# Optimization experiments

Hardware: AMD Instinct MI355X
Metric: run time of the kernel (lower is better)

Reference implementation:

```python
import jax, jax.numpy as jnp
import numpy as np

F_DIM = 128
H_DIM = 64
N_NODES = 100000
N_EDGES = 1000000
BN_EPS = 1e-5

def setup_inputs() -> dict:
    key = jax.random.key(0)
    ks = jax.random.split(key, 10)
    x = jax.random.normal(ks[0], (N_NODES, F_DIM), dtype=jnp.float32)
    edges = jax.random.randint(ks[1], (2, N_EDGES), 0, N_NODES, dtype=jnp.int64)
    s_in = 1.0 / np.sqrt(2 * F_DIM)
    s_h = 1.0 / np.sqrt(H_DIM)
    W_in = jax.random.uniform(ks[2], (H_DIM, 2 * F_DIM), jnp.float32, -s_in, s_in)
    b_in = jax.random.uniform(ks[3], (H_DIM,), jnp.float32, -s_in, s_in)
    W_h = jax.random.uniform(ks[4], (H_DIM, H_DIM), jnp.float32, -s_h, s_h)
    b_h = jax.random.uniform(ks[5], (H_DIM,), jnp.float32, -s_h, s_h)
    gamma = jnp.ones((H_DIM,), jnp.float32)
    beta = jnp.zeros((H_DIM,), jnp.float32)
    W_out = jax.random.uniform(ks[6], (1, H_DIM), jnp.float32, -s_h, s_h)
    b_out = jax.random.uniform(ks[7], (1,), jnp.float32, -s_h, s_h)
    return {"x": x, "edges": edges, "W_in": W_in, "b_in": b_in,
            "W_h": W_h, "b_h": b_h, "gamma": gamma, "beta": beta,
            "W_out": W_out, "b_out": b_out}

def reference(x, edges, W_in, b_in, W_h, b_h, gamma, beta, W_out, b_out):
    # gather node pair features and concat -> [E, 2F]
    ef = jnp.concatenate((x[edges[0]], x[edges[1]]), axis=1)
    h = jax.nn.relu(ef @ W_in.T + b_in)          # [E, H]
    h = h @ W_h.T + b_h                           # hidden linear
    # BatchNorm1d in training mode: batch stats over edge dim (biased var)
    mean = jnp.mean(h, axis=0)
    var = jnp.mean((h - mean) ** 2, axis=0)
    h = (h - mean) * jax.lax.rsqrt(var + BN_EPS) * gamma + beta
    h = jax.nn.relu(h)
    edge_scores = (h @ W_out.T + b_out).squeeze(-1)  # [E]
    return edge_scores
```

## Files before the change

### kernel.cpp

```cpp
#include <hip/hip_runtime.h>
#include <hip/hip_bf16.h>

#define N_NODES 100000
#define N_EDGES 1000000
#define BN_EPS 1e-5f
#define N_CHUNKS (N_EDGES / 64)

typedef __attribute__((ext_vector_type(8))) short bf16x8;
typedef __attribute__((ext_vector_type(4))) float f32x4;


__device__ __forceinline__ unsigned pk2(float a, float b) {
  unsigned ua = __builtin_bit_cast(unsigned, a);
  unsigned ub = __builtin_bit_cast(unsigned, b);
  ua += 0x7fffu + ((ua >> 16) & 1u);
  ub += 0x7fffu + ((ub >> 16) & 1u);
  return (ua >> 16) | (ub & 0xffff0000u);
}

__device__ __forceinline__ bf16x8 pack8(float4 v0, float4 v1) {
  uint4 u = make_uint4(pk2(v0.x, v0.y), pk2(v0.z, v0.w), pk2(v1.x, v1.y), pk2(v1.z, v1.w));
  return __builtin_bit_cast(bf16x8, u);
}

__global__ __launch_bounds__(64) void k_probe(const unsigned* __restrict__ eu,
                                              int* __restrict__ flag) {
  if (threadIdx.x == 0) {
    unsigned acc = 0;
#pragma unroll
    for (int i = 1; i < 64; i += 2) acc |= eu[i];
    *flag = (acc == 0) ? 1 : 0;
  }
}

__global__ __launch_bounds__(256) void k1_mfma(
    const float* __restrict__ x, const float* __restrict__ W_in,
    const float* __restrict__ b_in, __hip_bfloat16* __restrict__ A,
    float* __restrict__ stats) {
  const int t = threadIdx.x;
  if (blockIdx.x == 0 && t < 128) stats[t] = 0.f;
  const int lane = t & 63;
  const int w = t >> 6;
  const int l15 = lane & 15, l4 = lane >> 4;
  const int nb = blockIdx.x * 128 + (w >> 1) * 64;
  const int cb = (w & 1) * 64;

  bf16x8 wfrag[4][4];
#pragma unroll
  for (int ct = 0; ct < 4; ++ct) {
#pragma unroll
    for (int kk = 0; kk < 4; ++kk) {
      const float* wp = W_in + (16 * ct + l15) * 256 + (cb ? 128 : 0) + 32 * kk + 8 * l4;
      wfrag[ct][kk] = pack8(*(const float4*)wp, *(const float4*)(wp + 4));
    }
  }
  f32x4 acc[4][4];
#pragma unroll
  for (int nt = 0; nt < 4; ++nt)
#pragma unroll
    for (int ct = 0; ct < 4; ++ct)
      acc[nt][ct] = (f32x4){0.f, 0.f, 0.f, 0.f};

#pragma unroll
  for (int nt = 0; nt < 4; ++nt) {
    int node = nb + 16 * nt + l15;
    node = node < N_NODES ? node : N_NODES - 1;
    const float* xr = x + (size_t)node * 128 + 8 * l4;
#pragma unroll
    for (int kk = 0; kk < 4; ++kk) {
      const bf16x8 xf = pack8(*(const float4*)(xr + 32 * kk), *(const float4*)(xr + 32 * kk + 4));
#pragma unroll
      for (int ct = 0; ct < 4; ++ct)
        acc[nt][ct] = __builtin_amdgcn_mfma_f32_16x16x32_bf16(wfrag[ct][kk], xf, acc[nt][ct], 0, 0, 0);
    }
  }

  float4 bv[4];
#pragma unroll
  for (int ct = 0; ct < 4; ++ct)
    bv[ct] = cb ? make_float4(0.f, 0.f, 0.f, 0.f) : *(const float4*)(b_in + 16 * ct + 4 * l4);
#pragma unroll
  for (int nt = 0; nt < 4; ++nt) {
    const int node = nb + 16 * nt + l15;
    if (node < N_NODES) {
      __hip_bfloat16* ap = A + (size_t)node * 128 + cb + 4 * l4;
#pragma unroll
      for (int ct = 0; ct < 4; ++ct) {
        uint2 u;
        u.x = pk2(acc[nt][ct][0] + bv[ct].x, acc[nt][ct][1] + bv[ct].y);
        u.y = pk2(acc[nt][ct][2] + bv[ct].z, acc[nt][ct][3] + bv[ct].w);
        *(uint2*)(ap + 16 * ct) = u;
      }
    }
  }
}


__device__ __forceinline__ void stage_wh(const float* __restrict__ W_h, uint4* btile) {
  const int t = threadIdx.x;
#pragma unroll
  for (int rep = 0; rep < 2; ++rep) {
    const int idx = t + rep * 256;
    const int row = idx >> 3, c = idx & 7;
    const float* wp = W_h + row * 64 + c * 8;
    const float4 w0 = *(const float4*)wp;
    const float4 w1 = *(const float4*)(wp + 4);
    btile[row * 8 + (c ^ (row & 7))] =
        make_uint4(pk2(w0.x, w0.y), pk2(w0.z, w0.w), pk2(w1.x, w1.y), pk2(w1.z, w1.w));
  }
}

__device__ __forceinline__ void stage_h1(const __hip_bfloat16* __restrict__ As,
                                         const __hip_bfloat16* __restrict__ Ad,
                                         uint4* mytile, int lane) {
  const uint4* pa = (const uint4*)As;
  const uint4* pd = (const uint4*)Ad;
#pragma unroll
  for (int c = 0; c < 8; ++c) {
    const uint4 a = pa[c], d = pd[c];
    uint4 r;
    const unsigned* aw = (const unsigned*)&a;
    const unsigned* dw = (const unsigned*)&d;
    unsigned* rw = (unsigned*)&r;
#pragma unroll
    for (int q = 0; q < 4; ++q) {
      const float alo = __builtin_bit_cast(float, aw[q] << 16);
      const float ahi = __builtin_bit_cast(float, aw[q] & 0xffff0000u);
      const float dlo = __builtin_bit_cast(float, dw[q] << 16);
      const float dhi = __builtin_bit_cast(float, dw[q] & 0xffff0000u);
      rw[q] = pk2(fmaxf(alo + dlo, 0.f), fmaxf(ahi + dhi, 0.f));
    }
    mytile[lane * 8 + (c ^ (lane & 7))] = r;
  }
}

__global__ __launch_bounds__(256) void k2_stats(
    const __hip_bfloat16* __restrict__ A, const void* __restrict__ edges,
    const int* __restrict__ flag, const float* __restrict__ W_h,
    float* __restrict__ stats) {
  __shared__ uint4 tiles[4][64 * 8];
  __shared__ uint4 btile[64 * 8];
  const int lane = threadIdx.x & 63;
  const int wid = threadIdx.x >> 6;
  const int l15 = lane & 15, l4 = lane >> 4, lsw = l15 & 7;
  uint4* mytile = tiles[wid];
  stage_wh(W_h, btile);
  __syncthreads();
  bf16x8 bfr[4][2];
#pragma unroll
  for (int nt = 0; nt < 4; ++nt)
#pragma unroll
    for (int kk = 0; kk < 2; ++kk)
      bfr[nt][kk] = __builtin_bit_cast(bf16x8,
          btile[(nt * 16 + l15) * 8 + ((kk * 4 + l4) ^ lsw)]);

  const int is64 = *flag;
  const long long* e64 = (const long long*)edges;
  const int* e32 = (const int*)edges;
  float vs[4] = {0.f, 0.f, 0.f, 0.f};
  float vq[4] = {0.f, 0.f, 0.f, 0.f};
  const int gwave = blockIdx.x * 4 + wid;
  const int nwaves = gridDim.x * 4;
  for (int chunk = gwave; chunk < N_CHUNKS; chunk += nwaves) {
    const int e = chunk * 64 + lane;
    int s, d;
    if (is64) { s = (int)e64[e]; d = (int)e64[N_EDGES + e]; }
    else      { s = e32[e];      d = e32[N_EDGES + e]; }
    stage_h1(A + (size_t)s * 128, A + (size_t)d * 128 + 64, mytile, lane);
    asm volatile("s_waitcnt lgkmcnt(0)" ::: "memory");
    __builtin_amdgcn_sched_barrier(0);
#pragma unroll
    for (int mt = 0; mt < 4; ++mt) {
      const int arow = (mt * 16 + l15) * 8;
      const bf16x8 a0 = __builtin_bit_cast(bf16x8, mytile[arow + ((l4) ^ lsw)]);
      const bf16x8 a1 = __builtin_bit_cast(bf16x8, mytile[arow + ((4 + l4) ^ lsw)]);
#pragma unroll
      for (int nt = 0; nt < 4; ++nt) {
        f32x4 cacc = {0.f, 0.f, 0.f, 0.f};
        cacc = __builtin_amdgcn_mfma_f32_16x16x32_bf16(a0, bfr[nt][0], cacc, 0, 0, 0);
        cacc = __builtin_amdgcn_mfma_f32_16x16x32_bf16(a1, bfr[nt][1], cacc, 0, 0, 0);
#pragma unroll
        for (int j = 0; j < 4; ++j) {
          vs[nt] += cacc[j];
          vq[nt] += cacc[j] * cacc[j];
        }
      }
    }
  }
#pragma unroll
  for (int nt = 0; nt < 4; ++nt) {
    float s1 = vs[nt], s2 = vq[nt];
    s1 += __shfl_xor(s1, 16, 64); s1 += __shfl_xor(s1, 32, 64);
    s2 += __shfl_xor(s2, 16, 64); s2 += __shfl_xor(s2, 32, 64);
    if (lane < 16) {
      atomicAdd(&stats[lane + 16 * nt], s1);
      atomicAdd(&stats[64 + lane + 16 * nt], s2);
    }
  }
}

__global__ __launch_bounds__(64) void k3_finalize(
    const float* __restrict__ stats, const float* __restrict__ gamma,
    const float* __restrict__ beta, float* __restrict__ ss) {
  const int c = threadIdx.x;
  if (c < 64) {
    const float inv_e = 1.f / (float)N_EDGES;
    const float mg = stats[c] * inv_e;
    const float var = stats[64 + c] * inv_e - mg * mg;
    const float scale = gamma[c] * rsqrtf(var + BN_EPS);
    ss[c] = scale;
    ss[64 + c] = beta[c] - scale * mg;
  }
}

__global__ __launch_bounds__(256) void k4_out(
    const __hip_bfloat16* __restrict__ A, const void* __restrict__ edges,
    const int* __restrict__ flag, const float* __restrict__ W_h,
    const float* __restrict__ ss, const float* __restrict__ W_out,
    const float* __restrict__ b_out, float* __restrict__ out) {
  __shared__ uint4 tiles[4][64 * 8];
  __shared__ uint4 btile[64 * 8];
  const int lane = threadIdx.x & 63;
  const int wid = threadIdx.x >> 6;
  const int l15 = lane & 15, l4 = lane >> 4, lsw = l15 & 7;
  uint4* mytile = tiles[wid];
  stage_wh(W_h, btile);
  __syncthreads();
  bf16x8 bfr[4][2];
#pragma unroll
  for (int nt = 0; nt < 4; ++nt)
#pragma unroll
    for (int kk = 0; kk < 2; ++kk)
      bfr[nt][kk] = __builtin_bit_cast(bf16x8,
          btile[(nt * 16 + l15) * 8 + ((kk * 4 + l4) ^ lsw)]);
  float scl[4], shf[4], wo[4];
#pragma unroll
  for (int nt = 0; nt < 4; ++nt) {
    scl[nt] = ss[l15 + 16 * nt];
    shf[nt] = ss[64 + l15 + 16 * nt];
    wo[nt] = W_out[l15 + 16 * nt];
  }
  const float bo = b_out[0];
  const int is64 = *flag;
  const long long* e64 = (const long long*)edges;
  const int* e32 = (const int*)edges;
  const int gwave = blockIdx.x * 4 + wid;
  const int nwaves = gridDim.x * 4;
  for (int chunk = gwave; chunk < N_CHUNKS; chunk += nwaves) {
    const int e = chunk * 64 + lane;
    int s, d;
    if (is64) { s = (int)e64[e]; d = (int)e64[N_EDGES + e]; }
    else      { s = e32[e];      d = e32[N_EDGES + e]; }
    stage_h1(A + (size_t)s * 128, A + (size_t)d * 128 + 64, mytile, lane);
    asm volatile("s_waitcnt lgkmcnt(0)" ::: "memory");
    __builtin_amdgcn_sched_barrier(0);
#pragma unroll
    for (int mt = 0; mt < 4; ++mt) {
      const int arow = (mt * 16 + l15) * 8;
      const bf16x8 a0 = __builtin_bit_cast(bf16x8, mytile[arow + ((l4) ^ lsw)]);
      const bf16x8 a1 = __builtin_bit_cast(bf16x8, mytile[arow + ((4 + l4) ^ lsw)]);
      float t0 = 0.f, t1 = 0.f, t2 = 0.f, t3 = 0.f;
#pragma unroll
      for (int nt = 0; nt < 4; ++nt) {
        f32x4 cacc = {0.f, 0.f, 0.f, 0.f};
        cacc = __builtin_amdgcn_mfma_f32_16x16x32_bf16(a0, bfr[nt][0], cacc, 0, 0, 0);
        cacc = __builtin_amdgcn_mfma_f32_16x16x32_bf16(a1, bfr[nt][1], cacc, 0, 0, 0);
        t0 += fmaxf(fmaf(cacc[0], scl[nt], shf[nt]), 0.f) * wo[nt];
        t1 += fmaxf(fmaf(cacc[1], scl[nt], shf[nt]), 0.f) * wo[nt];
        t2 += fmaxf(fmaf(cacc[2], scl[nt], shf[nt]), 0.f) * wo[nt];
        t3 += fmaxf(fmaf(cacc[3], scl[nt], shf[nt]), 0.f) * wo[nt];
      }
      const int ebase = chunk * 64 + mt * 16 + 4 * l4;
#pragma unroll
      for (int j = 0; j < 4; ++j) {
        float r = (j == 0) ? t0 : (j == 1) ? t1 : (j == 2) ? t2 : t3;
        r += __shfl_xor(r, 1, 64);
        r += __shfl_xor(r, 2, 64);
        r += __shfl_xor(r, 4, 64);
        r += __shfl_xor(r, 8, 64);
        if (l15 == 0) out[ebase + j] = r + bo;
      }
    }
  }
}

extern "C" void kernel_launch(void* const* d_in, const int* in_sizes, int n_in,
                              void* d_out, int out_size, void* d_ws, size_t ws_size,
                              hipStream_t stream) {
  const float* x     = (const float*)d_in[0];
  const void*  edges = d_in[1];
  const float* W_in  = (const float*)d_in[2];
  const float* b_in  = (const float*)d_in[3];
  const float* W_h   = (const float*)d_in[4];
  const float* gamma = (const float*)d_in[6];
  const float* beta  = (const float*)d_in[7];
  const float* W_out = (const float*)d_in[8];
  const float* b_out = (const float*)d_in[9];
  float* out = (float*)d_out;

  char* base = (char*)d_ws;
  __hip_bfloat16* A = (__hip_bfloat16*)base;
  float* stats = (float*)(base + (size_t)N_NODES * 128 * sizeof(__hip_bfloat16));
  float* ss    = stats + 128;
  int*   flag  = (int*)(ss + 128);

  k_probe<<<1, 64, 0, stream>>>((const unsigned*)edges, flag);
  k1_mfma<<<782, 256, 0, stream>>>(x, W_in, b_in, A, stats);
  k2_stats<<<1024, 256, 0, stream>>>(A, edges, flag, W_h, stats);
  k3_finalize<<<1, 64, 0, stream>>>(stats, gamma, beta, ss);
  k4_out<<<1024, 256, 0, stream>>>(A, edges, flag, W_h, ss, W_out, b_out, out);
}
```

Before: 243.4 us.

## Materialize hidden pre-BN activations in fp16 and stream them in output pass

The stats kernel now writes the hidden-layer MFMA outputs to workspace as fp16, so the output kernel can stream them instead of re-gathering node rows and redoing the matmul. Both gather kernels also drop the shared-memory staging of the A fragments and W_h, loading them straight from global memory into MFMA registers. This trades a second random gather plus matmul for a 128 MB write and a read of the intermediate. It adds fp16 rounding of the pre-BN values, and it falls back to the old path when the workspace is too small.

New measurement: 219.9 us. -9.6%, faster.

```diff
diff --git a/kernel.cpp b/kernel.cpp
--- a/kernel.cpp
+++ b/kernel.cpp
@@ -1,5 +1,6 @@
 #include <hip/hip_runtime.h>
 #include <hip/hip_bf16.h>
+#include <hip/hip_fp16.h>
 
 #define N_NODES 100000
 #define N_EDGES 1000000
@@ -21,6 +22,33 @@
 __device__ __forceinline__ bf16x8 pack8(float4 v0, float4 v1) {
   uint4 u = make_uint4(pk2(v0.x, v0.y), pk2(v0.z, v0.w), pk2(v1.x, v1.y), pk2(v1.z, v1.w));
   return __builtin_bit_cast(bf16x8, u);
+}
+
+__device__ __forceinline__ bf16x8 frag_relu_add(uint4 a, uint4 d) {
+  uint4 r;
+  const unsigned* aw = (const unsigned*)&a;
+  const unsigned* dw = (const unsigned*)&d;
+  unsigned* rw = (unsigned*)&r;
+#pragma unroll
+  for (int q = 0; q < 4; ++q) {
+    const float alo = __builtin_bit_cast(float, aw[q] << 16);
+    const float ahi = __builtin_bit_cast(float, aw[q] & 0xffff0000u);
+    const float dlo = __builtin_bit_cast(float, dw[q] << 16);
+    const float dhi = __builtin_bit_cast(float, dw[q] & 0xffff0000u);
+    rw[q] = pk2(fmaxf(alo + dlo, 0.f), fmaxf(ahi + dhi, 0.f));
+  }
+  return __builtin_bit_cast(bf16x8, r);
+}
+
+__device__ __forceinline__ void load_bfr(const float* __restrict__ W_h, int l15, int l4,
+                                         bf16x8 bfr[4][2]) {
+#pragma unroll
+  for (int nt = 0; nt < 4; ++nt)
+#pragma unroll
+    for (int kk = 0; kk < 2; ++kk) {
+      const float* wp = W_h + (16 * nt + l15) * 64 + (kk * 4 + l4) * 8;
+      bfr[nt][kk] = pack8(*(const float4*)wp, *(const float4*)(wp + 4));
+    }
 }
 
 __global__ __launch_bounds__(64) void k_probe(const unsigned* __restrict__ eu,
@@ -95,94 +123,54 @@
   }
 }
 
-
-__device__ __forceinline__ void stage_wh(const float* __restrict__ W_h, uint4* btile) {
-  const int t = threadIdx.x;
-#pragma unroll
-  for (int rep = 0; rep < 2; ++rep) {
-    const int idx = t + rep * 256;
-    const int row = idx >> 3, c = idx & 7;
-    const float* wp = W_h + row * 64 + c * 8;
-    const float4 w0 = *(const float4*)wp;
-    const float4 w1 = *(const float4*)(wp + 4);
-    btile[row * 8 + (c ^ (row & 7))] =
-        make_uint4(pk2(w0.x, w0.y), pk2(w0.z, w0.w), pk2(w1.x, w1.y), pk2(w1.z, w1.w));
-  }
-}
-
-__device__ __forceinline__ void stage_h1(const __hip_bfloat16* __restrict__ As,
-                                         const __hip_bfloat16* __restrict__ Ad,
-                                         uint4* mytile, int lane) {
-  const uint4* pa = (const uint4*)As;
-  const uint4* pd = (const uint4*)Ad;
-#pragma unroll
-  for (int c = 0; c < 8; ++c) {
-    const uint4 a = pa[c], d = pd[c];
-    uint4 r;
-    const unsigned* aw = (const unsigned*)&a;
-    const unsigned* dw = (const unsigned*)&d;
-    unsigned* rw = (unsigned*)&r;
-#pragma unroll
-    for (int q = 0; q < 4; ++q) {
-      const float alo = __builtin_bit_cast(float, aw[q] << 16);
-      const float ahi = __builtin_bit_cast(float, aw[q] & 0xffff0000u);
-      const float dlo = __builtin_bit_cast(float, dw[q] << 16);
-      const float dhi = __builtin_bit_cast(float, dw[q] & 0xffff0000u);
-      rw[q] = pk2(fmaxf(alo + dlo, 0.f), fmaxf(ahi + dhi, 0.f));
-    }
-    mytile[lane * 8 + (c ^ (lane & 7))] = r;
-  }
-}
-
+template<bool STORE_G>
 __global__ __launch_bounds__(256) void k2_stats(
     const __hip_bfloat16* __restrict__ A, const void* __restrict__ edges,
     const int* __restrict__ flag, const float* __restrict__ W_h,
-    float* __restrict__ stats) {
-  __shared__ uint4 tiles[4][64 * 8];
-  __shared__ uint4 btile[64 * 8];
+    float* __restrict__ stats, __half* __restrict__ g) {
   const int lane = threadIdx.x & 63;
-  const int wid = threadIdx.x >> 6;
-  const int l15 = lane & 15, l4 = lane >> 4, lsw = l15 & 7;
-  uint4* mytile = tiles[wid];
-  stage_wh(W_h, btile);
-  __syncthreads();
+  const int l15 = lane & 15, l4 = lane >> 4;
   bf16x8 bfr[4][2];
-#pragma unroll
-  for (int nt = 0; nt < 4; ++nt)
-#pragma unroll
-    for (int kk = 0; kk < 2; ++kk)
-      bfr[nt][kk] = __builtin_bit_cast(bf16x8,
-          btile[(nt * 16 + l15) * 8 + ((kk * 4 + l4) ^ lsw)]);
+  load_bfr(W_h, l15, l4, bfr);
 
   const int is64 = *flag;
   const long long* e64 = (const long long*)edges;
   const int* e32 = (const int*)edges;
   float vs[4] = {0.f, 0.f, 0.f, 0.f};
   float vq[4] = {0.f, 0.f, 0.f, 0.f};
-  const int gwave = blockIdx.x * 4 + wid;
+  const int gwave = blockIdx.x * 4 + (threadIdx.x >> 6);
   const int nwaves = gridDim.x * 4;
   for (int chunk = gwave; chunk < N_CHUNKS; chunk += nwaves) {
-    const int e = chunk * 64 + lane;
-    int s, d;
-    if (is64) { s = (int)e64[e]; d = (int)e64[N_EDGES + e]; }
-    else      { s = e32[e];      d = e32[N_EDGES + e]; }
-    stage_h1(A + (size_t)s * 128, A + (size_t)d * 128 + 64, mytile, lane);
-    asm volatile("s_waitcnt lgkmcnt(0)" ::: "memory");
-    __builtin_amdgcn_sched_barrier(0);
+    const int base = chunk * 64;
 #pragma unroll
     for (int mt = 0; mt < 4; ++mt) {
-      const int arow = (mt * 16 + l15) * 8;
-      const bf16x8 a0 = __builtin_bit_cast(bf16x8, mytile[arow + ((l4) ^ lsw)]);
-      const bf16x8 a1 = __builtin_bit_cast(bf16x8, mytile[arow + ((4 + l4) ^ lsw)]);
+      const int eidx = base + mt * 16 + l15;
+      int s, d;
+      if (is64) { s = (int)e64[eidx]; d = (int)e64[N_EDGES + eidx]; }
+      else      { s = e32[eidx];      d = e32[N_EDGES + eidx]; }
+      const uint4* As = (const uint4*)(A + (size_t)s * 128);
+      const uint4* Ad = (const uint4*)(A + (size_t)d * 128 + 64);
+      const uint4 as0 = As[l4], as1 = As[4 + l4];
+      const uint4 ad0 = Ad[l4], ad1 = Ad[4 + l4];
+      const bf16x8 a0 = frag_relu_add(as0, ad0);
+      const bf16x8 a1 = frag_relu_add(as1, ad1);
 #pragma unroll
       for (int nt = 0; nt < 4; ++nt) {
-        f32x4 cacc = {0.f, 0.f, 0.f, 0.f};
-        cacc = __builtin_amdgcn_mfma_f32_16x16x32_bf16(a0, bfr[nt][0], cacc, 0, 0, 0);
-        cacc = __builtin_amdgcn_mfma_f32_16x16x32_bf16(a1, bfr[nt][1], cacc, 0, 0, 0);
+        f32x4 c = {0.f, 0.f, 0.f, 0.f};
+        c = __builtin_amdgcn_mfma_f32_16x16x32_bf16(a0, bfr[nt][0], c, 0, 0, 0);
+        c = __builtin_amdgcn_mfma_f32_16x16x32_bf16(a1, bfr[nt][1], c, 0, 0, 0);
+        if (STORE_G) {
+          const __half2 h0 = __floats2half2_rn(c[0], c[1]);
+          const __half2 h1 = __floats2half2_rn(c[2], c[3]);
+          uint2 u;
+          u.x = __builtin_bit_cast(unsigned, h0);
+          u.y = __builtin_bit_cast(unsigned, h1);
+          *(uint2*)(g + ((((size_t)chunk * 4 + mt) * 4 + nt) * 64 + lane) * 4) = u;
+        }
 #pragma unroll
         for (int j = 0; j < 4; ++j) {
-          vs[nt] += cacc[j];
-          vq[nt] += cacc[j] * cacc[j];
+          vs[nt] += c[j];
+          vq[nt] += c[j] * c[j];
         }
       }
     }
@@ -213,26 +201,59 @@
   }
 }
 
-__global__ __launch_bounds__(256) void k4_out(
+__global__ __launch_bounds__(256) void k4_stream(
+    const __half* __restrict__ g, const float* __restrict__ ss,
+    const float* __restrict__ W_out, const float* __restrict__ b_out,
+    float* __restrict__ out) {
+  const int lane = threadIdx.x & 63;
+  const int l15 = lane & 15, l4 = lane >> 4;
+  float scl[4], shf[4], wo[4];
+#pragma unroll
+  for (int nt = 0; nt < 4; ++nt) {
+    scl[nt] = ss[l15 + 16 * nt];
+    shf[nt] = ss[64 + l15 + 16 * nt];
+    wo[nt] = W_out[l15 + 16 * nt];
+  }
+  const float bo = b_out[0];
+  const int gwave = blockIdx.x * 4 + (threadIdx.x >> 6);
+  const int nwaves = gridDim.x * 4;
+  for (int chunk = gwave; chunk < N_CHUNKS; chunk += nwaves) {
+#pragma unroll
+    for (int mt = 0; mt < 4; ++mt) {
+      float t0 = 0.f, t1 = 0.f, t2 = 0.f, t3 = 0.f;
+#pragma unroll
+      for (int nt = 0; nt < 4; ++nt) {
+        const uint2 u = *(const uint2*)(g + ((((size_t)chunk * 4 + mt) * 4 + nt) * 64 + lane) * 4);
+        const __half2 h0 = __builtin_bit_cast(__half2, u.x);
+        const __half2 h1 = __builtin_bit_cast(__half2, u.y);
+        t0 += fmaxf(fmaf(__low2float(h0),  scl[nt], shf[nt]), 0.f) * wo[nt];
+        t1 += fmaxf(fmaf(__high2float(h0), scl[nt], shf[nt]), 0.f) * wo[nt];
+        t2 += fmaxf(fmaf(__low2float(h1),  scl[nt], shf[nt]), 0.f) * wo[nt];
+        t3 += fmaxf(fmaf(__high2float(h1), scl[nt], shf[nt]), 0.f) * wo[nt];
+      }
+      const int ebase = chunk * 64 + mt * 16 + 4 * l4;
+#pragma unroll
+      for (int j = 0; j < 4; ++j) {
+        float r = (j == 0) ? t0 : (j == 1) ? t1 : (j == 2) ? t2 : t3;
+        r += __shfl_xor(r, 1, 64);
+        r += __shfl_xor(r, 2, 64);
+        r += __shfl_xor(r, 4, 64);
+        r += __shfl_xor(r, 8, 64);
+        if (l15 == 0) out[ebase + j] = r + bo;
+      }
+    }
+  }
+}
+
+__global__ __launch_bounds__(256) void k4_gather(
     const __hip_bfloat16* __restrict__ A, const void* __restrict__ edges,
     const int* __restrict__ flag, const float* __restrict__ W_h,
     const float* __restrict__ ss, const float* __restrict__ W_out,
     const float* __restrict__ b_out, float* __restrict__ out) {
-  __shared__ uint4 tiles[4][64 * 8];
-  __shared__ uint4 btile[64 * 8];
   const int lane = threadIdx.x & 63;
-  const int wid = threadIdx.x >> 6;
-  const int l15 = lane & 15, l4 = lane >> 4, lsw = l15 & 7;
-  uint4* mytile = tiles[wid];
-  stage_wh(W_h, btile);
-  __syncthreads();
+  const int l15 = lane & 15, l4 = lane >> 4;
   bf16x8 bfr[4][2];
-#pragma unroll
-  for (int nt = 0; nt < 4; ++nt)
-#pragma unroll
-    for (int kk = 0; kk < 2; ++kk)
-      bfr[nt][kk] = __builtin_bit_cast(bf16x8,
-          btile[(nt * 16 + l15) * 8 + ((kk * 4 + l4) ^ lsw)]);
+  load_bfr(W_h, l15, l4, bfr);
   float scl[4], shf[4], wo[4];
 #pragma unroll
   for (int nt = 0; nt < 4; ++nt) {
@@ -244,33 +265,32 @@
   const int is64 = *flag;
   const long long* e64 = (const long long*)edges;
   const int* e32 = (const int*)edges;
-  const int gwave = blockIdx.x * 4 + wid;
+  const int gwave = blockIdx.x * 4 + (threadIdx.x >> 6);
   const int nwaves = gridDim.x * 4;
   for (int chunk = gwave; chunk < N_CHUNKS; chunk += nwaves) {
-    const int e = chunk * 64 + lane;
-    int s, d;
-    if (is64) { s = (int)e64[e]; d = (int)e64[N_EDGES + e]; }
-    else      { s = e32[e];      d = e32[N_EDGES + e]; }
-    stage_h1(A + (size_t)s * 128, A + (size_t)d * 128 + 64, mytile, lane);
-    asm volatile("s_waitcnt lgkmcnt(0)" ::: "memory");
-    __builtin_amdgcn_sched_barrier(0);
+    const int base = chunk * 64;
 #pragma unroll
     for (int mt = 0; mt < 4; ++mt) {
-      const int arow = (mt * 16 + l15) * 8;
-      const bf16x8 a0 = __builtin_bit_cast(bf16x8, mytile[arow + ((l4) ^ lsw)]);
-      const bf16x8 a1 = __builtin_bit_cast(bf16x8, mytile[arow + ((4 + l4) ^ lsw)]);
+      const int eidx = base + mt * 16 + l15;
+      int s, d;
+      if (is64) { s = (int)e64[eidx]; d = (int)e64[N_EDGES + eidx]; }
+      else      { s = e32[eidx];      d = e32[N_EDGES + eidx]; }
+      const uint4* As = (const uint4*)(A + (size_t)s * 128);
+      const uint4* Ad = (const uint4*)(A + (size_t)d * 128 + 64);
+      const bf16x8 a0 = frag_relu_add(As[l4], Ad[l4]);
+      const bf16x8 a1 = frag_relu_add(As[4 + l4], Ad[4 + l4]);
       float t0 = 0.f, t1 = 0.f, t2 = 0.f, t3 = 0.f;
 #pragma unroll
       for (int nt = 0; nt < 4; ++nt) {
-        f32x4 cacc = {0.f, 0.f, 0.f, 0.f};
-        cacc = __builtin_amdgcn_mfma_f32_16x16x32_bf16(a0, bfr[nt][0], cacc, 0, 0, 0);
-        cacc = __builtin_amdgcn_mfma_f32_16x16x32_bf16(a1, bfr[nt][1], cacc, 0, 0, 0);
-        t0 += fmaxf(fmaf(cacc[0], scl[nt], shf[nt]), 0.f) * wo[nt];
-        t1 += fmaxf(fmaf(cacc[1], scl[nt], shf[nt]), 0.f) * wo[nt];
-        t2 += fmaxf(fmaf(cacc[2], scl[nt], shf[nt]), 0.f) * wo[nt];
-        t3 += fmaxf(fmaf(cacc[3], scl[nt], shf[nt]), 0.f) * wo[nt];
-      }
-      const int ebase = chunk * 64 + mt * 16 + 4 * l4;
+        f32x4 c = {0.f, 0.f, 0.f, 0.f};
+        c = __builtin_amdgcn_mfma_f32_16x16x32_bf16(a0, bfr[nt][0], c, 0, 0, 0);
+        c = __builtin_amdgcn_mfma_f32_16x16x32_bf16(a1, bfr[nt][1], c, 0, 0, 0);
+        t0 += fmaxf(fmaf(c[0], scl[nt], shf[nt]), 0.f) * wo[nt];
+        t1 += fmaxf(fmaf(c[1], scl[nt], shf[nt]), 0.f) * wo[nt];
+        t2 += fmaxf(fmaf(c[2], scl[nt], shf[nt]), 0.f) * wo[nt];
+        t3 += fmaxf(fmaf(c[3], scl[nt], shf[nt]), 0.f) * wo[nt];
+      }
+      const int ebase = base + mt * 16 + 4 * l4;
 #pragma unroll
       for (int j = 0; j < 4; ++j) {
         float r = (j == 0) ? t0 : (j == 1) ? t1 : (j == 2) ? t2 : t3;
@@ -300,13 +320,23 @@
 
   char* base = (char*)d_ws;
   __hip_bfloat16* A = (__hip_bfloat16*)base;
-  float* stats = (float*)(base + (size_t)N_NODES * 128 * sizeof(__hip_bfloat16));
+  const size_t offStats = (size_t)N_NODES * 128 * sizeof(__hip_bfloat16);
+  float* stats = (float*)(base + offStats);
   float* ss    = stats + 128;
   int*   flag  = (int*)(ss + 128);
+  const size_t offG = offStats + 4096;
+  __half* g = (__half*)(base + offG);
+  const bool use_g = ws_size >= offG + (size_t)N_EDGES * 64 * sizeof(__half);
 
   k_probe<<<1, 64, 0, stream>>>((const unsigned*)edges, flag);
   k1_mfma<<<782, 256, 0, stream>>>(x, W_in, b_in, A, stats);
-  k2_stats<<<1024, 256, 0, stream>>>(A, edges, flag, W_h, stats);
-  k3_finalize<<<1, 64, 0, stream>>>(stats, gamma, beta, ss);
-  k4_out<<<1024, 256, 0, stream>>>(A, edges, flag, W_h, ss, W_out, b_out, out);
-}
+  if (use_g) {
+    k2_stats<true><<<1024, 256, 0, stream>>>(A, edges, flag, W_h, stats, g);
+    k3_finalize<<<1, 64, 0, stream>>>(stats, gamma, beta, ss);
+    k4_stream<<<1024, 256, 0, stream>>>(g, ss, W_out, b_out, out);
+  } else {
+    k2_stats<false><<<1024, 256, 0, stream>>>(A, edges, flag, W_h, stats, g);
+    k3_finalize<<<1, 64, 0, stream>>>(stats, gamma, beta, ss);
+    k4_gather<<<1024, 256, 0, stream>>>(A, edges, flag, W_h, ss, W_out, b_out, out);
+  }
+}
```
